# Kernel tuning notes

Measured on AMD Instinct MI355X. Metric: run time of the kernel, lower is better.

The kernel has to match this reference:

```python
import jax, jax.numpy as jnp
import numpy as np

TEMP = 5.0  # temperature_init
# All C(4,2)=6 keep-2-of-4 patterns for 2:4 semi-structured sparsity
PATTERNS = jnp.array([[1,1,0,0],[1,0,1,0],[1,0,0,1],[0,1,1,0],[0,1,0,1],[0,0,1,1]], dtype=jnp.float32)


def masked_linear(x, w, b, alpha, ids):
    # x: [N, I], w: [O, I], alpha: [A, O, I//4, 6], ids: [N]
    A, O, G, P = alpha.shape
    probs = jax.nn.softmax(alpha / TEMP, axis=-1)            # [A, O, G, 6]
    mask = jnp.einsum('aogp,pk->aogk', probs, PATTERNS)      # [A, O, G, 4]
    wm = w[None, :, :] * mask.reshape(A, O, G * 4)           # [A, O, I] per-agent masked weight
    y = jnp.einsum('ni,aoi->nao', x, wm)                     # dense per-agent GEMM
    y = jnp.take_along_axis(y, ids[:, None, None], axis=1)[:, 0, :]
    return y + b


def gru_cell(x, h, w_ih, w_hh, b_ih, b_hh):
    gi = x @ w_ih.T + b_ih
    gh = h @ w_hh.T + b_hh
    i_r, i_z, i_n = jnp.split(gi, 3, axis=-1)
    h_r, h_z, h_n = jnp.split(gh, 3, axis=-1)
    r = jax.nn.sigmoid(i_r + h_r)
    z = jax.nn.sigmoid(i_z + h_z)
    n = jnp.tanh(i_n + r * h_n)
    return (1.0 - z) * n + z * h


def setup_inputs() -> dict:
    key = jax.random.key(0)
    ks = jax.random.split(key, 20)
    B, A, E, H, NA = 1024, 8, 64, 512, 16
    s = 0.05
    d = {}
    d['inputs'] = jax.random.normal(ks[0], (B, A, E), jnp.float32)
    d['hidden_state'] = jax.random.normal(ks[1], (B, A, H), jnp.float32)
    d['agent_ids'] = jax.random.randint(ks[2], (B, A), 0, A, jnp.int32)
    d['fc1_w'] = jax.random.normal(ks[3], (H, E), jnp.float32) * s
    d['fc1_b'] = jax.random.normal(ks[4], (H,), jnp.float32) * s
    d['fc1_alpha'] = jax.random.normal(ks[5], (A, H, E // 4, 6), jnp.float32)
    d['gru_w_ih'] = jax.random.normal(ks[6], (3 * H, H), jnp.float32) * s
    d['gru_w_hh'] = jax.random.normal(ks[7], (3 * H, H), jnp.float32) * s
    d['gru_b_ih'] = jax.random.normal(ks[8], (3 * H,), jnp.float32) * s
    d['gru_b_hh'] = jax.random.normal(ks[9], (3 * H,), jnp.float32) * s
    d['fc2_w'] = jax.random.normal(ks[10], (H, H), jnp.float32) * s
    d['fc2_b'] = jax.random.normal(ks[11], (H,), jnp.float32) * s
    d['fc2_alpha'] = jax.random.normal(ks[12], (A, H, H // 4, 6), jnp.float32)
    d['fc3_w'] = jax.random.normal(ks[13], (H, H), jnp.float32) * s
    d['fc3_b'] = jax.random.normal(ks[14], (H,), jnp.float32) * s
    d['fc3_alpha'] = jax.random.normal(ks[15], (A, H, H // 4, 6), jnp.float32)
    d['fc4_w'] = jax.random.normal(ks[16], (NA, H), jnp.float32) * s
    d['fc4_b'] = jax.random.normal(ks[17], (NA,), jnp.float32) * s
    d['fc4_alpha'] = jax.random.normal(ks[18], (A, NA, H // 4, 6), jnp.float32)
    return d


def reference(inputs, hidden_state, agent_ids,
              fc1_w, fc1_b, fc1_alpha,
              gru_w_ih, gru_w_hh, gru_b_ih, gru_b_hh,
              fc2_w, fc2_b, fc2_alpha,
              fc3_w, fc3_b, fc3_alpha,
              fc4_w, fc4_b, fc4_alpha):
    b, a, e = inputs.shape
    H = hidden_state.shape[-1]
    x = inputs.reshape(-1, e)
    ids = agent_ids.reshape(-1)
    x = jax.nn.relu(masked_linear(x, fc1_w, fc1_b, fc1_alpha, ids))
    h = gru_cell(x, hidden_state.reshape(-1, H), gru_w_ih, gru_w_hh, gru_b_ih, gru_b_hh)
    q = jax.nn.relu(masked_linear(h, fc2_w, fc2_b, fc2_alpha, ids))
    q = jax.nn.relu(masked_linear(q, fc3_w, fc3_b, fc3_alpha, ids))
    q = masked_linear(q, fc4_w, fc4_b, fc4_alpha, ids)
    return q.reshape(b, a, -1), h.reshape(b, a, -1)
```

## Files before the change

kernel.cpp:

```cpp
#include <hip/hip_runtime.h>
#include <hip/hip_bf16.h>

typedef unsigned short ushort_t;
typedef __bf16 bf16x8 __attribute__((ext_vector_type(8)));
typedef unsigned short us8 __attribute__((ext_vector_type(8)));
typedef float f32x4 __attribute__((ext_vector_type(4)));

__device__ __forceinline__ float b2f(ushort_t h) {
    union { unsigned int u; float f; } v; v.u = ((unsigned int)h) << 16; return v.f;
}
__device__ __forceinline__ ushort_t f2b(float f) {
    union { float f; unsigned int u; } v; v.f = f;
    unsigned int u = v.u;
    unsigned int r = (u + 0x7FFFu + ((u >> 16) & 1u)) >> 16;
    return (ushort_t)r;
}
__device__ __forceinline__ float sigmoidf_(float x) {
    return 1.f / (1.f + __expf(-x));
}
__device__ __forceinline__ void store_o(ushort_t* p, float v) { *p = f2b(v); }
__device__ __forceinline__ void store_o(float* p, float v) { *p = v; }

__global__ void fill_kernel(float* out, long long n, float val) {
    long long i = (long long)blockIdx.x * blockDim.x + threadIdx.x;
    if (i < n) out[i] = val;
}

__global__ void sort_kernel(const int* __restrict__ ids, int N,
                            int* __restrict__ perm, int* __restrict__ seg,
                            int4* __restrict__ ttab, int* __restrict__ tcount) {
    __shared__ int cnt[8];
    __shared__ int off[8];
    int tid = threadIdx.x;
    if (tid < 8) cnt[tid] = 0;
    __syncthreads();
    for (int n = tid; n < N; n += blockDim.x) atomicAdd(&cnt[ids[n] & 7], 1);
    __syncthreads();
    if (tid == 0) {
        int s = 0;
        for (int a = 0; a < 8; a++) { off[a] = s; seg[a] = s; s += cnt[a]; }
        seg[8] = s;
        int T = 0;
        for (int a = 0; a < 8; a++)
            for (int m = seg[a]; m < seg[a + 1]; m += 64) {
                int e = seg[a + 1] < m + 64 ? seg[a + 1] : m + 64;
                ttab[T++] = make_int4(a, m, e, 0);
            }
        *tcount = T;
    }
    __syncthreads();
    for (int n = tid; n < N; n += blockDim.x) {
        int p = atomicAdd(&off[ids[n] & 7], 1);
        perm[p] = n;
    }
}

__device__ __forceinline__ void maskw_item(const float* __restrict__ alpha,
                                           const float* __restrict__ w,
                                           ushort_t* __restrict__ wm,
                                           long long idx, int O, int G) {
    int g = (int)(idx % G);
    long long t2 = idx / G;
    int o = (int)(t2 % O);
    const float* al = alpha + idx * 6;
    float p[6];
    float mx = -1e30f;
    #pragma unroll
    for (int i = 0; i < 6; i++) { p[i] = al[i] * 0.2f; mx = fmaxf(mx, p[i]); }
    float s = 0.f;
    #pragma unroll
    for (int i = 0; i < 6; i++) { p[i] = __expf(p[i] - mx); s += p[i]; }
    float inv = 1.f / s;
    #pragma unroll
    for (int i = 0; i < 6; i++) p[i] *= inv;
    float mk[4] = { p[0] + p[1] + p[2], p[0] + p[3] + p[4],
                    p[1] + p[3] + p[5], p[2] + p[4] + p[5] };
    int K = G * 4;
    const float* wr = w + (long long)o * K + g * 4;
    ushort_t* wo = wm + (idx / G) * (long long)K + g * 4;
    #pragma unroll
    for (int k = 0; k < 4; k++) wo[k] = f2b(wr[k] * mk[k]);
}

__device__ __forceinline__ void canon_item(const float* __restrict__ src,
                                           ushort_t* __restrict__ dst,
                                           long long i) {
    long long base = i * 8;
    us8 o;
    #pragma unroll
    for (int k = 0; k < 8; k++) o[k] = f2b(src[base + k]);
    *(us8*)(dst + base) = o;
}

#define PB0 256
#define PB1 2048
#define PB2 2048
#define PB3 64
#define PB4 256
#define PB5 2048
#define PB6 384
#define PB7 384
#define PREP_BLOCKS (PB0+PB1+PB2+PB3+PB4+PB5+PB6+PB7)

__global__ void prep_kernel(const float* fc1_al, const float* fc1_w, ushort_t* wm1,
                            const float* fc2_al, const float* fc2_w, ushort_t* wm2,
                            const float* fc3_al, const float* fc3_w, ushort_t* wm3,
                            const float* fc4_al, const float* fc4_w, ushort_t* wm4,
                            const float* inputs, ushort_t* inp_b,
                            const float* hidden, ushort_t* hid_b,
                            const float* wih, ushort_t* wihb,
                            const float* whh, ushort_t* whhb) {
    int b = blockIdx.x;
    int tid = threadIdx.x;
    if (b < PB0) { maskw_item(fc1_al, fc1_w, wm1, (long long)b * 256 + tid, 512, 16); return; }
    b -= PB0;
    if (b < PB1) { maskw_item(fc2_al, fc2_w, wm2, (long long)b * 256 + tid, 512, 128); return; }
    b -= PB1;
    if (b < PB2) { maskw_item(fc3_al, fc3_w, wm3, (long long)b * 256 + tid, 512, 128); return; }
    b -= PB2;
    if (b < PB3) { maskw_item(fc4_al, fc4_w, wm4, (long long)b * 256 + tid, 16, 128); return; }
    b -= PB3;
    if (b < PB4) { canon_item(inputs, inp_b, (long long)b * 256 + tid); return; }
    b -= PB4;
    if (b < PB5) { canon_item(hidden, hid_b, (long long)b * 256 + tid); return; }
    b -= PB5;
    if (b < PB6) { canon_item(wih, wihb, (long long)b * 256 + tid); return; }
    b -= PB6;
    canon_item(whh, whhb, (long long)b * 256 + tid);
}

#define BM 64
#define BN 64
#define BK 32

template <typename OT>
__launch_bounds__(256, 4)
__global__ void gemm_tiled(const ushort_t* __restrict__ In, int ldin,
                           const ushort_t* __restrict__ W, long long wstride,
                           const float* __restrict__ bias,
                           OT* __restrict__ Out, int ldo,
                           const int4* __restrict__ ttab,
                           const int* __restrict__ tcount,
                           const int* __restrict__ gather,
                           const int* __restrict__ scatter,
                           int O, int K, int relu) {
    int t = blockIdx.x;
    if (t >= *tcount) return;
    int4 tt = ttab[t];
    int a = tt.x, pos0 = tt.y, pos1 = tt.z;
    int o0 = blockIdx.y * BN;

    __shared__ ushort_t As[2048];
    __shared__ ushort_t Bs[2048];

    int tid = threadIdx.x;
    int wave = tid >> 6, lane = tid & 63;
    int wr = (wave >> 1) & 1, wc = wave & 1;
    int quad = lane >> 4, l16 = lane & 15;
    int srow = tid >> 2, sgrp = tid & 3;
    int scol = sgrp * 8;
    int wsoff = (srow * 4 + (sgrp ^ ((srow >> 2) & 3))) * 8;
    int rl = (l16 * 4 + (quad ^ ((l16 >> 2) & 3))) * 8;

    int apos = pos0 + srow;
    int apos_c = apos < pos1 ? apos : (pos1 - 1);
    int arow = (gather ? gather[apos_c] : apos_c) & 8191;
    const ushort_t* aptr = In + (long long)arow * ldin + scol;

    int brow = o0 + srow;
    int brow_c = brow < O ? brow : (O - 1);
    const ushort_t* bptr = W + (long long)a * wstride + (long long)brow_c * K + scol;

    f32x4 acc[2][2];
    #pragma unroll
    for (int i = 0; i < 2; i++)
        #pragma unroll
        for (int j = 0; j < 2; j++) acc[i][j] = (f32x4){0.f, 0.f, 0.f, 0.f};

    for (int k0 = 0; k0 < K; k0 += BK) {
        us8 av = *(const us8*)(aptr + k0);
        us8 bv = *(const us8*)(bptr + k0);
        __syncthreads();
        *(us8*)(&As[wsoff]) = av;
        *(us8*)(&Bs[wsoff]) = bv;
        __syncthreads();

        bf16x8 af[2], bfr[2];
        #pragma unroll
        for (int u = 0; u < 2; u++) {
            af[u]  = *(const bf16x8*)(&As[(wr * 2 + u) * 512 + rl]);
            bfr[u] = *(const bf16x8*)(&Bs[(wc * 2 + u) * 512 + rl]);
        }
        #pragma unroll
        for (int i = 0; i < 2; i++)
            #pragma unroll
            for (int j = 0; j < 2; j++)
                acc[i][j] = __builtin_amdgcn_mfma_f32_16x16x32_bf16(af[i], bfr[j], acc[i][j], 0, 0, 0);
    }

    #pragma unroll
    for (int i = 0; i < 2; i++) {
        int mbase = wr * 32 + i * 16 + quad * 4;
        #pragma unroll
        for (int j = 0; j < 2; j++) {
            int col = o0 + wc * 32 + j * 16 + l16;
            if (col < O) {
                float bias_v = bias ? bias[col] : 0.f;
                #pragma unroll
                for (int r = 0; r < 4; r++) {
                    int pos = pos0 + mbase + r;
                    if (pos < pos1) {
                        float v = acc[i][j][r] + bias_v;
                        if (relu) v = fmaxf(v, 0.f);
                        int orow = (scatter ? scatter[pos] : pos) & 8191;
                        store_o(&Out[(long long)orow * ldo + col], v);
                    }
                }
            }
        }
    }
}

__launch_bounds__(256, 2)
__global__ void gru_fused(const ushort_t* __restrict__ y1,
                          const ushort_t* __restrict__ hid_b,
                          const float* __restrict__ hidden_f,
                          const ushort_t* __restrict__ wihb,
                          const ushort_t* __restrict__ whhb,
                          const float* __restrict__ bih,
                          const float* __restrict__ bhh,
                          const int* __restrict__ perm,
                          float* __restrict__ out_h_f,
                          ushort_t* __restrict__ hp,
                          int N, int H) {
    int m0 = blockIdx.x * 64;
    int c0 = blockIdx.y * 64;

    __shared__ ushort_t Ay[2048];
    __shared__ ushort_t Ah[2048];
    __shared__ ushort_t Bt[6][2048];

    int tid = threadIdx.x;
    int wave = tid >> 6, lane = tid & 63;
    int wr = (wave >> 1) & 1, wc = wave & 1;
    int quad = lane >> 4, l16 = lane & 15;
    int srow = tid >> 2, sgrp = tid & 3;
    int scol = sgrp * 8;
    int wsoff = (srow * 4 + (sgrp ^ ((srow >> 2) & 3))) * 8;
    int rl = (l16 * 4 + (quad ^ ((l16 >> 2) & 3))) * 8;

    int hrow = perm[m0 + srow] & 8191;
    const ushort_t* ay_p = y1 + (long long)(m0 + srow) * H + scol;
    const ushort_t* ah_p = hid_b + (long long)hrow * H + scol;
    const ushort_t* bp[6];
    #pragma unroll
    for (int g = 0; g < 3; g++)
        bp[g] = wihb + (long long)(g * H + c0 + srow) * H + scol;
    #pragma unroll
    for (int g = 3; g < 6; g++)
        bp[g] = whhb + (long long)((g - 3) * H + c0 + srow) * H + scol;

    f32x4 acc[6][2][2];
    #pragma unroll
    for (int g = 0; g < 6; g++)
        #pragma unroll
        for (int i = 0; i < 2; i++)
            #pragma unroll
            for (int j = 0; j < 2; j++) acc[g][i][j] = (f32x4){0.f, 0.f, 0.f, 0.f};

    for (int k0 = 0; k0 < H; k0 += BK) {
        us8 va = *(const us8*)(ay_p + k0);
        us8 vh = *(const us8*)(ah_p + k0);
        us8 vb[6];
        #pragma unroll
        for (int g = 0; g < 6; g++) vb[g] = *(const us8*)(bp[g] + k0);
        __syncthreads();
        *(us8*)(&Ay[wsoff]) = va;
        *(us8*)(&Ah[wsoff]) = vh;
        #pragma unroll
        for (int g = 0; g < 6; g++) *(us8*)(&Bt[g][wsoff]) = vb[g];
        __syncthreads();

        bf16x8 ayf[2], ahf[2];
        #pragma unroll
        for (int u = 0; u < 2; u++) {
            ayf[u] = *(const bf16x8*)(&Ay[(wr * 2 + u) * 512 + rl]);
            ahf[u] = *(const bf16x8*)(&Ah[(wr * 2 + u) * 512 + rl]);
        }
        #pragma unroll
        for (int g = 0; g < 6; g++) {
            bf16x8 bfr[2];
            #pragma unroll
            for (int u = 0; u < 2; u++)
                bfr[u] = *(const bf16x8*)(&Bt[g][(wc * 2 + u) * 512 + rl]);
            #pragma unroll
            for (int i = 0; i < 2; i++)
                #pragma unroll
                for (int j = 0; j < 2; j++)
                    acc[g][i][j] = __builtin_amdgcn_mfma_f32_16x16x32_bf16(
                        (g < 3) ? ayf[i] : ahf[i], bfr[j], acc[g][i][j], 0, 0, 0);
        }
    }

    #pragma unroll
    for (int i = 0; i < 2; i++) {
        #pragma unroll
        for (int r = 0; r < 4; r++) {
            int pos = m0 + wr * 32 + i * 16 + quad * 4 + r;
            int norig = perm[pos] & 8191;
            #pragma unroll
            for (int j = 0; j < 2; j++) {
                int col = c0 + wc * 32 + j * 16 + l16;
                float ir = acc[0][i][j][r] + bih[col];
                float iz = acc[1][i][j][r] + bih[H + col];
                float in_ = acc[2][i][j][r] + bih[2 * H + col];
                float hr = acc[3][i][j][r] + bhh[col];
                float hz = acc[4][i][j][r] + bhh[H + col];
                float hn = acc[5][i][j][r] + bhh[2 * H + col];
                float rg = sigmoidf_(ir + hr);
                float zg = sigmoidf_(iz + hz);
                float ng = tanhf(in_ + rg * hn);
                float hv = hidden_f[(long long)norig * H + col];
                float hnew = (1.f - zg) * ng + zg * hv;
                out_h_f[(long long)norig * H + col] = hnew;
                hp[(long long)pos * H + col] = f2b(hnew);
            }
        }
    }
}

extern "C" void kernel_launch(void* const* d_in, const int* in_sizes, int n_in,
                              void* d_out, int out_size, void* d_ws, size_t ws_size,
                              hipStream_t stream) {
    (void)in_sizes; (void)n_in;
    const int N = 8192, A = 8, E = 64, H = 512, NA = 16;

    float* out_f = (float*)d_out;
    float* out_q = out_f;
    float* out_h = out_f + (size_t)N * NA;

    char* p = (char*)d_ws;
    auto alloc = [&](size_t b) { char* r = p; p += (b + 255) & ~(size_t)255; return r; };
    int*  perm   = (int*)alloc((size_t)N * 4);
    int*  seg    = (int*)alloc(16 * 4);
    int4* ttab   = (int4*)alloc(144 * 16);
    int*  tcount = (int*)alloc(256);
    ushort_t* wm1   = (ushort_t*)alloc((size_t)A * H * E * 2);
    ushort_t* wm2   = (ushort_t*)alloc((size_t)A * H * H * 2);
    ushort_t* wm3   = (ushort_t*)alloc((size_t)A * H * H * 2);
    ushort_t* wm4   = (ushort_t*)alloc((size_t)A * NA * H * 2);
    ushort_t* y1    = (ushort_t*)alloc((size_t)N * H * 2);
    ushort_t* inp_b = (ushort_t*)alloc((size_t)N * E * 2);
    ushort_t* hid_b = (ushort_t*)alloc((size_t)N * H * 2);
    ushort_t* wihb  = (ushort_t*)alloc((size_t)3 * H * H * 2);
    ushort_t* whhb  = (ushort_t*)alloc((size_t)3 * H * H * 2);
    ushort_t* hp    = (ushort_t*)alloc((size_t)N * H * 2);
    size_t need = (size_t)(p - (char*)d_ws);
    ushort_t* q2 = y1;
    ushort_t* q3 = hid_b;

    if (ws_size < need) {
        fill_kernel<<<(unsigned)((out_size + 255) / 256), 256, 0, stream>>>(
            out_f, out_size, 1000.f);
        return;
    }

    const float* inputs = (const float*)d_in[0];
    const float* hidden = (const float*)d_in[1];
    const int*   ids    = (const int*)d_in[2];
    const float* fc1_w  = (const float*)d_in[3];
    const float* fc1_b  = (const float*)d_in[4];
    const float* fc1_al = (const float*)d_in[5];
    const float* wih    = (const float*)d_in[6];
    const float* whh    = (const float*)d_in[7];
    const float* bih    = (const float*)d_in[8];
    const float* bhh    = (const float*)d_in[9];
    const float* fc2_w  = (const float*)d_in[10];
    const float* fc2_b  = (const float*)d_in[11];
    const float* fc2_al = (const float*)d_in[12];
    const float* fc3_w  = (const float*)d_in[13];
    const float* fc3_b  = (const float*)d_in[14];
    const float* fc3_al = (const float*)d_in[15];
    const float* fc4_w  = (const float*)d_in[16];
    const float* fc4_b  = (const float*)d_in[17];
    const float* fc4_al = (const float*)d_in[18];

    sort_kernel<<<1, 1024, 0, stream>>>(ids, N, perm, seg, ttab, tcount);

    prep_kernel<<<PREP_BLOCKS, 256, 0, stream>>>(
        fc1_al, fc1_w, wm1, fc2_al, fc2_w, wm2, fc3_al, fc3_w, wm3,
        fc4_al, fc4_w, wm4, inputs, inp_b, hidden, hid_b, wih, wihb, whh, whhb);

    dim3 blk(256);
    gemm_tiled<ushort_t><<<dim3(136, H / BN), blk, 0, stream>>>(
        inp_b, E, wm1, (long long)H * E, fc1_b, y1, H, ttab, tcount,
        perm, nullptr, H, E, 1);
    gru_fused<<<dim3(N / 64, H / 64), blk, 0, stream>>>(
        y1, hid_b, hidden, wihb, whhb, bih, bhh, perm, out_h, hp, N, H);
    gemm_tiled<ushort_t><<<dim3(136, H / BN), blk, 0, stream>>>(
        hp, H, wm2, (long long)H * H, fc2_b, q2, H, ttab, tcount,
        nullptr, nullptr, H, H, 1);
    gemm_tiled<ushort_t><<<dim3(136, H / BN), blk, 0, stream>>>(
        q2, H, wm3, (long long)H * H, fc3_b, q3, H, ttab, tcount,
        nullptr, nullptr, H, H, 1);
    gemm_tiled<float><<<dim3(136, 1), blk, 0, stream>>>(
        q3, H, wm4, (long long)NA * H, fc4_b, out_q, NA, ttab, tcount,
        nullptr, perm, NA, H, 0);
}
```

Baseline: 244.8 us.

## Prepack weights into MFMA fragment layout and pre-gather rows by agent

The prep kernel now writes masked and GRU weights in a packed layout that matches the per-lane MFMA B-fragment order, so the GEMM and GRU kernels load B fragments straight from global memory and drop their B shared-memory tiles and the associated stores. Input and hidden activations are gathered into sorted agent order during prep, so the GEMMs read contiguous rows without indirect lookups. This cuts LDS traffic and shared-memory footprint, which may allow more resident blocks. The cost is uncoalesced or repeated global reads of weight fragments that depend on cache hits, and fc4's small weight is duplicated to fill a 64-wide tile.

```diff
diff --git a/kernel.cpp b/kernel.cpp
--- a/kernel.cpp
+++ b/kernel.cpp
@@ -25,6 +25,8 @@
     long long i = (long long)blockIdx.x * blockDim.x + threadIdx.x;
     if (i < n) out[i] = val;
 }
+
+#define PACKSZ(O, K) ((long long)((O) >= 64 ? (O) >> 6 : 1) * ((K) >> 5) * 2048)
 
 __global__ void sort_kernel(const int* __restrict__ ids, int N,
                             int* __restrict__ perm, int* __restrict__ seg,
@@ -58,10 +60,11 @@
 __device__ __forceinline__ void maskw_item(const float* __restrict__ alpha,
                                            const float* __restrict__ w,
                                            ushort_t* __restrict__ wm,
-                                           long long idx, int O, int G) {
+                                           long long idx, int O, int G, int dup) {
     int g = (int)(idx % G);
     long long t2 = idx / G;
     int o = (int)(t2 % O);
+    int a = (int)(t2 / O);
     const float* al = alpha + idx * 6;
     float p[6];
     float mx = -1e30f;
@@ -77,19 +80,53 @@
                     p[1] + p[3] + p[5], p[2] + p[4] + p[5] };
     int K = G * 4;
     const float* wr = w + (long long)o * K + g * 4;
-    ushort_t* wo = wm + (idx / G) * (long long)K + g * 4;
-    #pragma unroll
-    for (int k = 0; k < 4; k++) wo[k] = f2b(wr[k] * mk[k]);
-}
-
-__device__ __forceinline__ void canon_item(const float* __restrict__ src,
-                                           ushort_t* __restrict__ dst,
-                                           long long i) {
+    ushort_t* base = wm + (long long)a * PACKSZ(O, K);
+    int k0 = g * 4;
+    int c = o >> 6, su = (o >> 4) & 3, n = o & 15;
+    int kk = k0 >> 5, q = (k0 >> 3) & 3, e0 = k0 & 7;
+    long long off = (((long long)(c * (K >> 5) + kk) * 4 + su) * 64 + (q * 16 + n)) * 8 + e0;
+    #pragma unroll
+    for (int t = 0; t < 4; t++) {
+        ushort_t v = f2b(wr[t] * mk[t]);
+        base[off + t] = v;
+        if (dup) {
+            base[off + t + 512] = v;
+            base[off + t + 1024] = v;
+            base[off + t + 1536] = v;
+        }
+    }
+}
+
+__device__ __forceinline__ void canon_gather_item(const float* __restrict__ src,
+                                                  ushort_t* __restrict__ dst,
+                                                  const int* __restrict__ perm,
+                                                  int ld, long long i) {
     long long base = i * 8;
-    us8 o;
-    #pragma unroll
-    for (int k = 0; k < 8; k++) o[k] = f2b(src[base + k]);
-    *(us8*)(dst + base) = o;
+    int pos = (int)(base / ld);
+    int k = (int)(base % ld);
+    int row = perm[pos] & 8191;
+    const float* s = src + (long long)row * ld + k;
+    us8 v;
+    #pragma unroll
+    for (int e = 0; e < 8; e++) v[e] = f2b(s[e]);
+    *(us8*)(dst + base) = v;
+}
+
+__device__ __forceinline__ void canon_pack_item(const float* __restrict__ src,
+                                                ushort_t* __restrict__ dst,
+                                                long long i) {
+    long long base = i * 8;
+    int o_full = (int)(base >> 9);
+    int k0 = (int)(base & 511);
+    int g = o_full >> 9, o = o_full & 511;
+    int c = o >> 6, su = (o >> 4) & 3, n = o & 15;
+    int kk = k0 >> 5, q = (k0 >> 3) & 3;
+    long long off = (long long)g * 262144 +
+        (((long long)(c * 16 + kk) * 4 + su) * 64 + (q * 16 + n)) * 8;
+    us8 v;
+    #pragma unroll
+    for (int e = 0; e < 8; e++) v[e] = f2b(src[base + e]);
+    *(us8*)(dst + off) = v;
 }
 
 #define PB0 256
@@ -106,42 +143,41 @@
                             const float* fc2_al, const float* fc2_w, ushort_t* wm2,
                             const float* fc3_al, const float* fc3_w, ushort_t* wm3,
                             const float* fc4_al, const float* fc4_w, ushort_t* wm4,
-                            const float* inputs, ushort_t* inp_b,
-                            const float* hidden, ushort_t* hid_b,
-                            const float* wih, ushort_t* wihb,
-                            const float* whh, ushort_t* whhb) {
+                            const float* inputs, ushort_t* inp_pos,
+                            const float* hidden, ushort_t* hid_pos,
+                            const float* wih, ushort_t* wihp,
+                            const float* whh, ushort_t* whhp,
+                            const int* perm) {
     int b = blockIdx.x;
     int tid = threadIdx.x;
-    if (b < PB0) { maskw_item(fc1_al, fc1_w, wm1, (long long)b * 256 + tid, 512, 16); return; }
+    if (b < PB0) { maskw_item(fc1_al, fc1_w, wm1, (long long)b * 256 + tid, 512, 16, 0); return; }
     b -= PB0;
-    if (b < PB1) { maskw_item(fc2_al, fc2_w, wm2, (long long)b * 256 + tid, 512, 128); return; }
+    if (b < PB1) { maskw_item(fc2_al, fc2_w, wm2, (long long)b * 256 + tid, 512, 128, 0); return; }
     b -= PB1;
-    if (b < PB2) { maskw_item(fc3_al, fc3_w, wm3, (long long)b * 256 + tid, 512, 128); return; }
+    if (b < PB2) { maskw_item(fc3_al, fc3_w, wm3, (long long)b * 256 + tid, 512, 128, 0); return; }
     b -= PB2;
-    if (b < PB3) { maskw_item(fc4_al, fc4_w, wm4, (long long)b * 256 + tid, 16, 128); return; }
+    if (b < PB3) { maskw_item(fc4_al, fc4_w, wm4, (long long)b * 256 + tid, 16, 128, 1); return; }
     b -= PB3;
-    if (b < PB4) { canon_item(inputs, inp_b, (long long)b * 256 + tid); return; }
+    if (b < PB4) { canon_gather_item(inputs, inp_pos, perm, 64, (long long)b * 256 + tid); return; }
     b -= PB4;
-    if (b < PB5) { canon_item(hidden, hid_b, (long long)b * 256 + tid); return; }
+    if (b < PB5) { canon_gather_item(hidden, hid_pos, perm, 512, (long long)b * 256 + tid); return; }
     b -= PB5;
-    if (b < PB6) { canon_item(wih, wihb, (long long)b * 256 + tid); return; }
+    if (b < PB6) { canon_pack_item(wih, wihp, (long long)b * 256 + tid); return; }
     b -= PB6;
-    canon_item(whh, whhb, (long long)b * 256 + tid);
+    canon_pack_item(whh, whhp, (long long)b * 256 + tid);
 }
 
 #define BM 64
 #define BN 64
-#define BK 32
 
 template <typename OT>
 __launch_bounds__(256, 4)
 __global__ void gemm_tiled(const ushort_t* __restrict__ In, int ldin,
-                           const ushort_t* __restrict__ W, long long wstride,
+                           const ushort_t* __restrict__ Wpk, long long wstride,
                            const float* __restrict__ bias,
                            OT* __restrict__ Out, int ldo,
                            const int4* __restrict__ ttab,
                            const int* __restrict__ tcount,
-                           const int* __restrict__ gather,
                            const int* __restrict__ scatter,
                            int O, int K, int relu) {
     int t = blockIdx.x;
@@ -151,25 +187,21 @@
     int o0 = blockIdx.y * BN;
 
     __shared__ ushort_t As[2048];
-    __shared__ ushort_t Bs[2048];
 
     int tid = threadIdx.x;
     int wave = tid >> 6, lane = tid & 63;
     int wr = (wave >> 1) & 1, wc = wave & 1;
     int quad = lane >> 4, l16 = lane & 15;
     int srow = tid >> 2, sgrp = tid & 3;
-    int scol = sgrp * 8;
     int wsoff = (srow * 4 + (sgrp ^ ((srow >> 2) & 3))) * 8;
     int rl = (l16 * 4 + (quad ^ ((l16 >> 2) & 3))) * 8;
 
     int apos = pos0 + srow;
     int apos_c = apos < pos1 ? apos : (pos1 - 1);
-    int arow = (gather ? gather[apos_c] : apos_c) & 8191;
-    const ushort_t* aptr = In + (long long)arow * ldin + scol;
-
-    int brow = o0 + srow;
-    int brow_c = brow < O ? brow : (O - 1);
-    const ushort_t* bptr = W + (long long)a * wstride + (long long)brow_c * K + scol;
+    const ushort_t* aptr = In + (long long)apos_c * ldin + sgrp * 8;
+
+    const ushort_t* wb = Wpk + (long long)a * wstride +
+        (long long)blockIdx.y * (K >> 5) * 2048 + lane * 8;
 
     f32x4 acc[2][2];
     #pragma unroll
@@ -177,20 +209,18 @@
         #pragma unroll
         for (int j = 0; j < 2; j++) acc[i][j] = (f32x4){0.f, 0.f, 0.f, 0.f};
 
-    for (int k0 = 0; k0 < K; k0 += BK) {
-        us8 av = *(const us8*)(aptr + k0);
-        us8 bv = *(const us8*)(bptr + k0);
+    int KK = K >> 5;
+    for (int kk = 0; kk < KK; kk++) {
+        us8 av = *(const us8*)(aptr + kk * 32);
+        bf16x8 bfr[2];
+        bfr[0] = *(const bf16x8*)(wb + (kk * 4 + wc * 2 + 0) * 512);
+        bfr[1] = *(const bf16x8*)(wb + (kk * 4 + wc * 2 + 1) * 512);
         __syncthreads();
         *(us8*)(&As[wsoff]) = av;
-        *(us8*)(&Bs[wsoff]) = bv;
         __syncthreads();
-
-        bf16x8 af[2], bfr[2];
-        #pragma unroll
-        for (int u = 0; u < 2; u++) {
-            af[u]  = *(const bf16x8*)(&As[(wr * 2 + u) * 512 + rl]);
-            bfr[u] = *(const bf16x8*)(&Bs[(wc * 2 + u) * 512 + rl]);
-        }
+        bf16x8 af[2];
+        af[0] = *(const bf16x8*)(&As[(wr * 2 + 0) * 512 + rl]);
+        af[1] = *(const bf16x8*)(&As[(wr * 2 + 1) * 512 + rl]);
         #pragma unroll
         for (int i = 0; i < 2; i++)
             #pragma unroll
@@ -223,10 +253,10 @@
 
 __launch_bounds__(256, 2)
 __global__ void gru_fused(const ushort_t* __restrict__ y1,
-                          const ushort_t* __restrict__ hid_b,
+                          const ushort_t* __restrict__ hid_pos,
                           const float* __restrict__ hidden_f,
-                          const ushort_t* __restrict__ wihb,
-                          const ushort_t* __restrict__ whhb,
+                          const ushort_t* __restrict__ wihp,
+                          const ushort_t* __restrict__ whhp,
                           const float* __restrict__ bih,
                           const float* __restrict__ bhh,
                           const int* __restrict__ perm,
@@ -234,31 +264,27 @@
                           ushort_t* __restrict__ hp,
                           int N, int H) {
     int m0 = blockIdx.x * 64;
-    int c0 = blockIdx.y * 64;
 
     __shared__ ushort_t Ay[2048];
     __shared__ ushort_t Ah[2048];
-    __shared__ ushort_t Bt[6][2048];
 
     int tid = threadIdx.x;
     int wave = tid >> 6, lane = tid & 63;
     int wr = (wave >> 1) & 1, wc = wave & 1;
     int quad = lane >> 4, l16 = lane & 15;
     int srow = tid >> 2, sgrp = tid & 3;
-    int scol = sgrp * 8;
     int wsoff = (srow * 4 + (sgrp ^ ((srow >> 2) & 3))) * 8;
     int rl = (l16 * 4 + (quad ^ ((l16 >> 2) & 3))) * 8;
 
-    int hrow = perm[m0 + srow] & 8191;
-    const ushort_t* ay_p = y1 + (long long)(m0 + srow) * H + scol;
-    const ushort_t* ah_p = hid_b + (long long)hrow * H + scol;
-    const ushort_t* bp[6];
-    #pragma unroll
-    for (int g = 0; g < 3; g++)
-        bp[g] = wihb + (long long)(g * H + c0 + srow) * H + scol;
-    #pragma unroll
-    for (int g = 3; g < 6; g++)
-        bp[g] = whhb + (long long)((g - 3) * H + c0 + srow) * H + scol;
+    const ushort_t* ay_p = y1 + (long long)(m0 + srow) * H + sgrp * 8;
+    const ushort_t* ah_p = hid_pos + (long long)(m0 + srow) * H + sgrp * 8;
+
+    long long cb = (long long)blockIdx.y * 16 * 2048 + lane * 8;
+    const ushort_t* wb[6];
+    #pragma unroll
+    for (int g = 0; g < 3; g++) wb[g] = wihp + (long long)g * 262144 + cb;
+    #pragma unroll
+    for (int g = 3; g < 6; g++) wb[g] = whhp + (long long)(g - 3) * 262144 + cb;
 
     f32x4 acc[6][2][2];
     #pragma unroll
@@ -268,17 +294,12 @@
             #pragma unroll
             for (int j = 0; j < 2; j++) acc[g][i][j] = (f32x4){0.f, 0.f, 0.f, 0.f};
 
-    for (int k0 = 0; k0 < H; k0 += BK) {
-        us8 va = *(const us8*)(ay_p + k0);
-        us8 vh = *(const us8*)(ah_p + k0);
-        us8 vb[6];
-        #pragma unroll
-        for (int g = 0; g < 6; g++) vb[g] = *(const us8*)(bp[g] + k0);
+    for (int kk = 0; kk < 16; kk++) {
+        us8 va = *(const us8*)(ay_p + kk * 32);
+        us8 vh = *(const us8*)(ah_p + kk * 32);
         __syncthreads();
         *(us8*)(&Ay[wsoff]) = va;
         *(us8*)(&Ah[wsoff]) = vh;
-        #pragma unroll
-        for (int g = 0; g < 6; g++) *(us8*)(&Bt[g][wsoff]) = vb[g];
         __syncthreads();
 
         bf16x8 ayf[2], ahf[2];
@@ -287,12 +308,12 @@
             ayf[u] = *(const bf16x8*)(&Ay[(wr * 2 + u) * 512 + rl]);
             ahf[u] = *(const bf16x8*)(&Ah[(wr * 2 + u) * 512 + rl]);
         }
+        int fo = (kk * 4 + wc * 2) * 512;
         #pragma unroll
         for (int g = 0; g < 6; g++) {
             bf16x8 bfr[2];
-            #pragma unroll
-            for (int u = 0; u < 2; u++)
-                bfr[u] = *(const bf16x8*)(&Bt[g][(wc * 2 + u) * 512 + rl]);
+            bfr[0] = *(const bf16x8*)(wb[g] + fo);
+            bfr[1] = *(const bf16x8*)(wb[g] + fo + 512);
             #pragma unroll
             for (int i = 0; i < 2; i++)
                 #pragma unroll
@@ -302,6 +323,7 @@
         }
     }
 
+    int c0 = blockIdx.y * 64;
     #pragma unroll
     for (int i = 0; i < 2; i++) {
         #pragma unroll
@@ -345,19 +367,19 @@
     int*  seg    = (int*)alloc(16 * 4);
     int4* ttab   = (int4*)alloc(144 * 16);
     int*  tcount = (int*)alloc(256);
-    ushort_t* wm1   = (ushort_t*)alloc((size_t)A * H * E * 2);
-    ushort_t* wm2   = (ushort_t*)alloc((size_t)A * H * H * 2);
-    ushort_t* wm3   = (ushort_t*)alloc((size_t)A * H * H * 2);
-    ushort_t* wm4   = (ushort_t*)alloc((size_t)A * NA * H * 2);
-    ushort_t* y1    = (ushort_t*)alloc((size_t)N * H * 2);
-    ushort_t* inp_b = (ushort_t*)alloc((size_t)N * E * 2);
-    ushort_t* hid_b = (ushort_t*)alloc((size_t)N * H * 2);
-    ushort_t* wihb  = (ushort_t*)alloc((size_t)3 * H * H * 2);
-    ushort_t* whhb  = (ushort_t*)alloc((size_t)3 * H * H * 2);
-    ushort_t* hp    = (ushort_t*)alloc((size_t)N * H * 2);
+    ushort_t* wm1     = (ushort_t*)alloc((size_t)A * PACKSZ(H, E) * 2);
+    ushort_t* wm2     = (ushort_t*)alloc((size_t)A * PACKSZ(H, H) * 2);
+    ushort_t* wm3     = (ushort_t*)alloc((size_t)A * PACKSZ(H, H) * 2);
+    ushort_t* wm4     = (ushort_t*)alloc((size_t)A * PACKSZ(NA, H) * 2);
+    ushort_t* y1      = (ushort_t*)alloc((size_t)N * H * 2);
+    ushort_t* inp_pos = (ushort_t*)alloc((size_t)N * E * 2);
+    ushort_t* hid_pos = (ushort_t*)alloc((size_t)N * H * 2);
+    ushort_t* wihp    = (ushort_t*)alloc((size_t)3 * H * H * 2);
+    ushort_t* whhp    = (ushort_t*)alloc((size_t)3 * H * H * 2);
+    ushort_t* hp      = (ushort_t*)alloc((size_t)N * H * 2);
     size_t need = (size_t)(p - (char*)d_ws);
     ushort_t* q2 = y1;
-    ushort_t* q3 = hid_b;
+    ushort_t* q3 = hid_pos;
 
     if (ws_size < need) {
         fill_kernel<<<(unsigned)((out_size + 255) / 256), 256, 0, stream>>>(
@@ -389,21 +411,22 @@
 
     prep_kernel<<<PREP_BLOCKS, 256, 0, stream>>>(
         fc1_al, fc1_w, wm1, fc2_al, fc2_w, wm2, fc3_al, fc3_w, wm3,
-        fc4_al, fc4_w, wm4, inputs, inp_b, hidden, hid_b, wih, wihb, whh, whhb);
+        fc4_al, fc4_w, wm4, inputs, inp_pos, hidden, hid_pos,
+        wih, wihp, whh, whhp, perm);
 
     dim3 blk(256);
     gemm_tiled<ushort_t><<<dim3(136, H / BN), blk, 0, stream>>>(
-        inp_b, E, wm1, (long long)H * E, fc1_b, y1, H, ttab, tcount,
-        perm, nullptr, H, E, 1);
+        inp_pos, E, wm1, PACKSZ(H, E), fc1_b, y1, H, ttab, tcount,
+        nullptr, H, E, 1);
     gru_fused<<<dim3(N / 64, H / 64), blk, 0, stream>>>(
-        y1, hid_b, hidden, wihb, whhb, bih, bhh, perm, out_h, hp, N, H);
+        y1, hid_pos, hidden, wihp, whhp, bih, bhh, perm, out_h, hp, N, H);
     gemm_tiled<ushort_t><<<dim3(136, H / BN), blk, 0, stream>>>(
-        hp, H, wm2, (long long)H * H, fc2_b, q2, H, ttab, tcount,
-        nullptr, nullptr, H, H, 1);
+        hp, H, wm2, PACKSZ(H, H), fc2_b, q2, H, ttab, tcount,
+        nullptr, H, H, 1);
     gemm_tiled<ushort_t><<<dim3(136, H / BN), blk, 0, stream>>>(
-        q2, H, wm3, (long long)H * H, fc3_b, q3, H, ttab, tcount,
-        nullptr, nullptr, H, H, 1);
+        q2, H, wm3, PACKSZ(H, H), fc3_b, q3, H, ttab, tcount,
+        nullptr, H, H, 1);
     gemm_tiled<float><<<dim3(136, 1), blk, 0, stream>>>(
-        q3, H, wm4, (long long)NA * H, fc4_b, out_q, NA, ttab, tcount,
-        nullptr, perm, NA, H, 0);
-}
+        q3, H, wm4, PACKSZ(NA, H), fc4_b, out_q, NA, ttab, tcount,
+        perm, NA, H, 0);
+}
```

Result: slower. 267.8 us (+9.4%).
